# Kernel optimization log

Measured on AMD Instinct MI355X. Metric: run time of the kernel, lower is better.

## Reference

```python
import jax, jax.numpy as jnp
import numpy as np

N, B, F_DIM, K, DEG = 102400, 64, 64, 16, 8
E = N * DEG
PER_G = N // B  # equal-size graphs -> to_dense_batch is a reshape
EPS = 1e-15


def setup_inputs() -> dict:
    key = jax.random.key(0)
    k1, k2, k3, k4 = jax.random.split(key, 4)
    node_attr = jax.random.normal(k1, (N, F_DIM), dtype=jnp.float32)
    W = jax.random.normal(k2, (F_DIM, K), dtype=jnp.float32) * 0.1
    b = jnp.zeros((K,), dtype=jnp.float32)
    row = jax.random.randint(k3, (E,), 0, N)
    # receivers constrained to the sender's graph (block structure)
    col = (row // PER_G) * PER_G + jax.random.randint(k4, (E,), 0, PER_G)
    edge_index = jnp.stack([row, col]).astype(jnp.int32)
    batch = jnp.repeat(jnp.arange(B, dtype=jnp.int32), PER_G)
    return {"node_attr": node_attr, "W": W, "b": b,
            "edge_index": edge_index, "batch": batch, "num_graphs": B}


def reference(node_attr, W, b, edge_index, batch, num_graphs):
    n, f = node_attr.shape
    k = W.shape[1]
    per_g = n // num_graphs
    # selection = softmax(Linear(node_attr))            [N, K]
    sel = jax.nn.softmax(node_attr @ W + b, axis=-1)
    s = sel.reshape(num_graphs, per_g, k)               # to_dense_batch (equal graphs)
    row, col = edge_index[0], edge_index[1]
    # edge_pooling: outer product per edge, scatter-add by graph of sender
    assign_edge = sel[row][:, :, None] * sel[col][:, None, :]       # [E, K, K]
    dense_adj = jax.ops.segment_sum(assign_edge, batch[row], num_segments=num_graphs)  # [B, K, K]
    # normalize_adj (remove_self_loops=False)
    d = jnp.sqrt(dense_adj.sum(-1))[:, None, :] + EPS   # [B, 1, K]
    dense_adj = dense_adj / d / jnp.swapaxes(d, 1, 2)
    # mincut loss
    mincut_num = jnp.trace(dense_adj, axis1=1, axis2=2)             # [B]
    deg = jax.ops.segment_sum(jnp.ones((row.shape[0],), node_attr.dtype), row, num_segments=n)
    d_flat = deg.reshape(num_graphs, per_g)                          # [B, Nmax]
    # trace(S^T diag(d) S) = sum_n d_n * sum_k s_nk^2
    mincut_den = jnp.einsum('bn,bnk,bnk->b', d_flat, s, s)
    mincut_loss = jnp.mean(-(mincut_num / mincut_den))
    # orthogonality loss
    ss = jnp.einsum('bnk,bnl->bkl', s, s)                            # [B, K, K]
    ss_norm = jnp.linalg.norm(ss, axis=(-2, -1), keepdims=True)
    i_s = jnp.eye(k, dtype=ss.dtype)
    ortho = jnp.linalg.norm(ss / ss_norm - i_s / jnp.sqrt(jnp.asarray(k, ss.dtype)), axis=(-2, -1))
    ortho_loss = jnp.mean(ortho)
    # node_pooling: scatter of sel ⊗ node_attr by graph, flattened over (B, K)
    x = node_attr.reshape(num_graphs, per_g, f)
    cluster_node_attr = jnp.einsum('bnk,bnf->bkf', s, x).reshape(num_graphs * k, f)
    return cluster_node_attr, dense_adj, mincut_loss, ortho_loss
```

## Files before the change

kernel.cpp:

```cpp
#include <hip/hip_runtime.h>

#define F_DIMC 64
#define K_DIMC 16
#define NGRAPH 64
#define NXCD 8
#define SX_WAVES 8
#define SX_SPLIT 8
#define NB_SEL 400
#define NB_CHUNK 256
#define NB_ZERO 64
#define CHUNK_I4 800
#define ADJ_BLOCKS 256
#define ADJ_OFF (NGRAPH * K_DIMC * F_DIMC)
#define LOSS_OFF (ADJ_OFF + NGRAPH * K_DIMC * K_DIMC)
#define ZERO_BYTES 394240

typedef __attribute__((ext_vector_type(8))) short s16x8;
typedef __attribute__((ext_vector_type(4))) float f32x4;


__device__ inline unsigned short f2bf(float f) {
    unsigned u = __builtin_bit_cast(unsigned, f);
    u += 0x7fffu + ((u >> 16) & 1u);
    return (unsigned short)(u >> 16);
}

__global__ __launch_bounds__(256) void k_sel_hist(const float* __restrict__ node_attr,
                                                  const float* __restrict__ W,
                                                  const float* __restrict__ bias,
                                                  const int* __restrict__ row,
                                                  float* __restrict__ sel,
                                                  int* __restrict__ blockhist,
                                                  float4* __restrict__ zdst,
                                                  int N, int perG) {
    int t = threadIdx.x;
    if (blockIdx.x < NB_SEL) {
        __shared__ float sW[K_DIMC][F_DIMC];
        __shared__ float sb[K_DIMC];
        for (int idx = t; idx < F_DIMC * K_DIMC; idx += 256) {
            int f = idx / K_DIMC, k = idx % K_DIMC;
            sW[k][f] = W[idx];
        }
        if (t < K_DIMC) sb[t] = bias[t];
        __syncthreads();
        int n = blockIdx.x * 256 + t;
        if (n >= N) return;

        const float4* xr = (const float4*)(node_attr + (size_t)n * F_DIMC);
        float4 x[F_DIMC / 4];
#pragma unroll
        for (int f4 = 0; f4 < F_DIMC / 4; ++f4) x[f4] = xr[f4];

        float logits[K_DIMC];
#pragma unroll
        for (int k = 0; k < K_DIMC; ++k) {
            const float4* wk = (const float4*)&sW[k][0];
            float acc = sb[k];
#pragma unroll
            for (int f4 = 0; f4 < F_DIMC / 4; ++f4) {
                float4 w = wk[f4];
                acc += x[f4].x * w.x + x[f4].y * w.y + x[f4].z * w.z + x[f4].w * w.w;
            }
            logits[k] = acc;
        }
        float m = logits[0];
#pragma unroll
        for (int k = 1; k < K_DIMC; ++k) m = fmaxf(m, logits[k]);
        float sum = 0.f;
#pragma unroll
        for (int k = 0; k < K_DIMC; ++k) {
            float e = __expf(logits[k] - m);
            logits[k] = e;
            sum += e;
        }
        float inv = 1.f / sum;
        float4* sd = (float4*)(sel + (size_t)n * K_DIMC);
#pragma unroll
        for (int k4 = 0; k4 < K_DIMC / 4; ++k4) {
            float4 v;
            v.x = logits[4 * k4 + 0] * inv;
            v.y = logits[4 * k4 + 1] * inv;
            v.z = logits[4 * k4 + 2] * inv;
            v.w = logits[4 * k4 + 3] * inv;
            sd[k4] = v;
        }
    } else if (blockIdx.x < NB_SEL + NB_CHUNK) {
        __shared__ int lh[NGRAPH];
        int h = blockIdx.x - NB_SEL;
        if (t < NGRAPH) lh[t] = 0;
        __syncthreads();
        for (int i = t; i < CHUNK_I4; i += 256) {
            int4 r4 = ((const int4*)row)[h * CHUNK_I4 + i];
            atomicAdd(&lh[r4.x / perG], 1);
            atomicAdd(&lh[r4.y / perG], 1);
            atomicAdd(&lh[r4.z / perG], 1);
            atomicAdd(&lh[r4.w / perG], 1);
        }
        __syncthreads();
        if (t < NGRAPH) blockhist[h * NGRAPH + t] = lh[t];
    } else {
        int z = blockIdx.x - NB_SEL - NB_CHUNK;
        for (int i = z * 256 + t; i < ZERO_BYTES / 16; i += NB_ZERO * 256)
            zdst[i] = make_float4(0.f, 0.f, 0.f, 0.f);
    }
}

__global__ __launch_bounds__(256) void k_chunkscan(const int* __restrict__ blockhist,
                                                   int* __restrict__ chunkbase,
                                                   int* __restrict__ gtot) {
    int g = blockIdx.x;
    int t = threadIdx.x;
    int lane = t & 63;
    int wid = t >> 6;
    int v = blockhist[t * NGRAPH + g];
    int s = v;
#pragma unroll
    for (int d = 1; d < 64; d <<= 1) {
        int o = __shfl_up(s, d);
        if (lane >= d) s += o;
    }
    __shared__ int wsum[4];
    if (lane == 63) wsum[wid] = s;
    __syncthreads();
    int pre = 0;
#pragma unroll
    for (int w = 0; w < 4; ++w) pre += (w < wid) ? wsum[w] : 0;
    int incl = s + pre;
    chunkbase[t * NGRAPH + g] = incl - v;
    if (t == 255) gtot[g] = incl;
}

__global__ __launch_bounds__(256) void k_scatter(const int* __restrict__ row,
                                                 const int* __restrict__ col,
                                                 const int* __restrict__ gtot,
                                                 const int* __restrict__ chunkbase,
                                                 int* __restrict__ offsets,
                                                 uint2* __restrict__ sorted,
                                                 int perG) {
    __shared__ int base_[NGRAPH];
    __shared__ int lcnt[NGRAPH];
    int t = threadIdx.x;
    int h = blockIdx.x;
    if (t < 64) {
        int v = gtot[t];
        int s = v;
#pragma unroll
        for (int d = 1; d < 64; d <<= 1) {
            int o = __shfl_up(s, d);
            if (t >= d) s += o;
        }
        int offs = s - v;
        base_[t] = offs + chunkbase[h * NGRAPH + t];
        lcnt[t] = 0;
        if (h == 0) offsets[t] = offs;
    }
    __syncthreads();
    for (int i = t; i < CHUNK_I4; i += 256) {
        int e4 = h * CHUNK_I4 + i;
        int4 r4 = ((const int4*)row)[e4];
        int4 c4 = ((const int4*)col)[e4];
        int rr[4] = {r4.x, r4.y, r4.z, r4.w};
        int cc[4] = {c4.x, c4.y, c4.z, c4.w};
#pragma unroll
        for (int u = 0; u < 4; ++u) {
            int g = rr[u] / perG;
            int lpos = atomicAdd(&lcnt[g], 1);
            sorted[(size_t)base_[g] + lpos] = make_uint2((unsigned)rr[u], (unsigned)cc[u]);
        }
    }
}

__global__ __launch_bounds__(256) void k_adj(const uint2* __restrict__ sorted,
                                             const int* __restrict__ offsets,
                                             const int* __restrict__ gtot,
                                             const float* __restrict__ sel,
                                             float* __restrict__ dense_raw,
                                             float* __restrict__ den) {
    __shared__ unsigned short At[4][512];
    __shared__ unsigned short Bt[4][512];
    __shared__ float lacc[4][256];
    __shared__ float qred[4];
    int b = blockIdx.x;
    int xcd = b & (NXCD - 1);
    int idx = b >> 3;
    int g = xcd * (NGRAPH / NXCD) + (idx >> 2);
    int split = idx & 3;
    int t = threadIdx.x;
    int wid = t >> 6;
    int lane = t & 63;
    int m = lane & 15;
    int grp = lane >> 4;
    int half8 = (lane & 1) * 8;

    int start = offsets[g];
    int cnt = gtot[g];
    int wslot = split * 4 + wid;
    f32x4 acc = {0.f, 0.f, 0.f, 0.f};
    float qacc = 0.f;
    int nch = (cnt + 31) >> 5;
    for (int ch = wslot; ch < nch; ch += 16) {
        int e0 = ch << 5;
        int eIdx = e0 + (lane >> 1);
        s16x8 av8 = {0, 0, 0, 0, 0, 0, 0, 0};
        s16x8 bv8 = {0, 0, 0, 0, 0, 0, 0, 0};
        if (eIdx < cnt) {
            uint2 pr = sorted[start + eIdx];
            const float4* ra = (const float4*)(sel + (size_t)pr.x * K_DIMC + half8);
            float4 a0 = ra[0], a1 = ra[1];
            qacc += a0.x * a0.x + a0.y * a0.y + a0.z * a0.z + a0.w * a0.w
                  + a1.x * a1.x + a1.y * a1.y + a1.z * a1.z + a1.w * a1.w;
            av8[0] = (short)f2bf(a0.x); av8[1] = (short)f2bf(a0.y);
            av8[2] = (short)f2bf(a0.z); av8[3] = (short)f2bf(a0.w);
            av8[4] = (short)f2bf(a1.x); av8[5] = (short)f2bf(a1.y);
            av8[6] = (short)f2bf(a1.z); av8[7] = (short)f2bf(a1.w);
            const float4* rb = (const float4*)(sel + (size_t)pr.y * K_DIMC + half8);
            float4 b0 = rb[0], b1 = rb[1];
            bv8[0] = (short)f2bf(b0.x); bv8[1] = (short)f2bf(b0.y);
            bv8[2] = (short)f2bf(b0.z); bv8[3] = (short)f2bf(b0.w);
            bv8[4] = (short)f2bf(b1.x); bv8[5] = (short)f2bf(b1.y);
            bv8[6] = (short)f2bf(b1.z); bv8[7] = (short)f2bf(b1.w);
        }
        ((s16x8*)At[wid])[lane] = av8;
        ((s16x8*)Bt[wid])[lane] = bv8;
        s16x8 av, bv;
#pragma unroll
        for (int d = 0; d < 8; ++d) {
            int off = (8 * grp + d) * K_DIMC + m;
            av[d] = (short)At[wid][off];
            bv[d] = (short)Bt[wid][off];
        }
        acc = __builtin_amdgcn_mfma_f32_16x16x32_bf16(av, bv, acc, 0, 0, 0);
    }
#pragma unroll
    for (int d = 0; d < 4; ++d) {
        lacc[wid][(4 * grp + d) * K_DIMC + m] = acc[d];
    }
#pragma unroll
    for (int off = 32; off > 0; off >>= 1) qacc += __shfl_down(qacc, off);
    if (lane == 0) qred[wid] = qacc;
    __syncthreads();
    float s = lacc[0][t] + lacc[1][t] + lacc[2][t] + lacc[3][t];
    atomicAdd(dense_raw + g * 256 + t, s);
    if (t == 0) {
        atomicAdd(den + g, qred[0] + qred[1] + qred[2] + qred[3]);
    }
}

__global__ __launch_bounds__(512) void k_sx(const float* __restrict__ sel,
                                            const float* __restrict__ x,
                                            float* __restrict__ ssbuf,
                                            float* __restrict__ sxbuf, int perG) {
    int g = blockIdx.y;
    int wid = threadIdx.x >> 6;
    int wslot = blockIdx.x * SX_WAVES + wid;
    int lane = threadIdx.x & 63;
    int k = lane >> 2;
    int sub = lane & 3;
    int f0 = sub * 16;
    int j0 = sub * 4;
    float accss[4] = {0.f, 0.f, 0.f, 0.f};
    float accsx[16];
#pragma unroll
    for (int j = 0; j < 16; ++j) accsx[j] = 0.f;
    size_t base = (size_t)g * perG;
    int stride = SX_SPLIT * SX_WAVES;
#pragma unroll 2
    for (int nn = wslot; nn < perG; nn += stride) {
        size_t node = base + nn;
        float a = sel[node * K_DIMC + k];
        float4 s4 = *(const float4*)(sel + node * K_DIMC + j0);
        accss[0] += a * s4.x;
        accss[1] += a * s4.y;
        accss[2] += a * s4.z;
        accss[3] += a * s4.w;
        const float4* xv = (const float4*)(x + node * F_DIMC + f0);
#pragma unroll
        for (int j = 0; j < 4; ++j) {
            float4 v = xv[j];
            accsx[4 * j + 0] += a * v.x;
            accsx[4 * j + 1] += a * v.y;
            accsx[4 * j + 2] += a * v.z;
            accsx[4 * j + 3] += a * v.w;
        }
    }
    __shared__ float lsx[SX_WAVES][K_DIMC * F_DIMC];
    __shared__ float lss[SX_WAVES][256];
#pragma unroll
    for (int j4 = 0; j4 < 4; ++j4) {
        *(float4*)&lsx[wid][k * F_DIMC + f0 + 4 * j4] =
            make_float4(accsx[4 * j4], accsx[4 * j4 + 1], accsx[4 * j4 + 2], accsx[4 * j4 + 3]);
    }
    *(float4*)&lss[wid][k * K_DIMC + j0] = make_float4(accss[0], accss[1], accss[2], accss[3]);
    __syncthreads();
    for (int c = threadIdx.x; c < K_DIMC * F_DIMC; c += 512) {
        float s = 0.f;
#pragma unroll
        for (int w = 0; w < SX_WAVES; ++w) s += lsx[w][c];
        atomicAdd(sxbuf + (size_t)g * (K_DIMC * F_DIMC) + c, s);
    }
    if (threadIdx.x < 256) {
        int c = threadIdx.x;
        float s = 0.f;
#pragma unroll
        for (int w = 0; w < SX_WAVES; ++w) s += lss[w][c];
        atomicAdd(ssbuf + g * 256 + c, s);
    }
}

__global__ __launch_bounds__(256) void k_fin(const float* __restrict__ dense_raw,
                                             const float* __restrict__ ssbuf,
                                             const float* __restrict__ sxbuf,
                                             const float* __restrict__ den,
                                             float* __restrict__ lossws,
                                             int* __restrict__ donecnt,
                                             float* __restrict__ out) {
    int g = blockIdx.x;
    int c = threadIdx.x;
    int k = c >> 4, j = c & 15;
    int lane = threadIdx.x & 63;
    int wid = threadIdx.x >> 6;

    ((float4*)(out + (size_t)g * (K_DIMC * F_DIMC)))[c] =
        ((const float4*)(sxbuf + (size_t)g * (K_DIMC * F_DIMC)))[c];

    float a = dense_raw[g * 256 + c];
    float s = a;
    s += __shfl_xor(s, 1);
    s += __shfl_xor(s, 2);
    s += __shfl_xor(s, 4);
    s += __shfl_xor(s, 8);
    __shared__ float dvrow[K_DIMC];
    if (j == 0) dvrow[k] = sqrtf(s) + 1e-15f;
    __syncthreads();
    float v = a / (dvrow[k] * dvrow[j]);
    out[ADJ_OFF + g * 256 + c] = v;

    float ss = ssbuf[g * 256 + c];
    float tt = (k == j) ? v : 0.f;
    float n2 = ss * ss;
#pragma unroll
    for (int off = 32; off > 0; off >>= 1) {
        tt += __shfl_down(tt, off);
        n2 += __shfl_down(n2, off);
    }
    __shared__ float redt[4], redn[4];
    if (lane == 0) { redt[wid] = tt; redn[wid] = n2; }
    __syncthreads();
    float tr = redt[0] + redt[1] + redt[2] + redt[3];
    float nrm2 = redn[0] + redn[1] + redn[2] + redn[3];
    float invn = 1.f / sqrtf(nrm2);
    float d = ss * invn - ((k == j) ? 0.25f : 0.f);
    float o2 = d * d;
#pragma unroll
    for (int off = 32; off > 0; off >>= 1) o2 += __shfl_down(o2, off);
    __shared__ float redo[4];
    if (lane == 0) redo[wid] = o2;
    __syncthreads();
    if (threadIdx.x == 0) {
        float osum = redo[0] + redo[1] + redo[2] + redo[3];
        float og = sqrtf(osum);
        float mterm = -(tr / den[g]);
        atomicAdd(lossws + 0, mterm * (1.f / NGRAPH));
        atomicAdd(lossws + 1, og * (1.f / NGRAPH));
        __threadfence();
        int old = atomicAdd(donecnt, 1);
        if (old == NGRAPH - 1) {
            float l0 = atomicAdd(lossws + 0, 0.f);
            float l1 = atomicAdd(lossws + 1, 0.f);
            out[LOSS_OFF + 0] = l0;
            out[LOSS_OFF + 1] = l1;
        }
    }
}

extern "C" void kernel_launch(void* const* d_in, const int* in_sizes, int n_in,
                              void* d_out, int out_size, void* d_ws, size_t ws_size,
                              hipStream_t stream) {
    const float* node_attr = (const float*)d_in[0];
    const float* W = (const float*)d_in[1];
    const float* bias = (const float*)d_in[2];
    const int* edge_index = (const int*)d_in[3];
    int N = in_sizes[0] / F_DIMC;
    int E = in_sizes[3] / 2;
    int perG = N / NGRAPH;
    const int* row = edge_index;
    const int* col = edge_index + E;
    float* out = (float*)d_out;
    char* ws = (char*)d_ws;

    float* den = (float*)(ws + 0);
    int* donecnt = (int*)(ws + 256);
    float* lossws = (float*)(ws + 512);
    float* dense_raw = (float*)(ws + 1024);
    float* ssbuf = (float*)(ws + 66560);
    float* sxbuf = (float*)(ws + 132096);
    int* offsets = (int*)(ws + 394240);
    int* gtot = (int*)(ws + 394496);
    int* blockhist = (int*)(ws + 394752);
    int* chunkbase = (int*)(ws + 460288);
    float* sel = (float*)(ws + 525824);
    uint2* sorted = (uint2*)(ws + 7079424);

    k_sel_hist<<<NB_SEL + NB_CHUNK + NB_ZERO, 256, 0, stream>>>(node_attr, W, bias, row, sel,
                                                                blockhist, (float4*)ws, N, perG);
    k_chunkscan<<<NGRAPH, 256, 0, stream>>>(blockhist, chunkbase, gtot);
    k_scatter<<<NB_CHUNK, 256, 0, stream>>>(row, col, gtot, chunkbase, offsets,
                                            sorted, perG);
    k_adj<<<ADJ_BLOCKS, 256, 0, stream>>>(sorted, offsets, gtot, sel, dense_raw, den);
    k_sx<<<dim3(SX_SPLIT, NGRAPH), 512, 0, stream>>>(sel, node_attr, ssbuf, sxbuf, perG);
    k_fin<<<NGRAPH, 256, 0, stream>>>(dense_raw, ssbuf, sxbuf, den, lossws, donecnt, out);
}
```

Baseline: 85.97 us.

## Fuse node-pooling reduction into edge scatter kernel via heterogeneous blocks

Merges the S^T S / S^T X reduction kernel into the edge scatter kernel as additional block roles, interleaving one scatter block with four reduction blocks. This removes a kernel launch and lets the memory-bound reduction overlap with the atomic-heavy scatter. The reduction uses 256-thread blocks with twice as many splits and an XCD-aware graph mapping. Shared memory for both roles is allocated per block, which may reduce occupancy for the scatter blocks.

```diff
diff --git a/kernel.cpp b/kernel.cpp
--- a/kernel.cpp
+++ b/kernel.cpp
@@ -4,8 +4,7 @@
 #define K_DIMC 16
 #define NGRAPH 64
 #define NXCD 8
-#define SX_WAVES 8
-#define SX_SPLIT 8
+#define SX_SPLIT 16
 #define NB_SEL 400
 #define NB_CHUNK 256
 #define NB_ZERO 64
@@ -130,42 +129,104 @@
     if (t == 255) gtot[g] = incl;
 }
 
-__global__ __launch_bounds__(256) void k_scatter(const int* __restrict__ row,
-                                                 const int* __restrict__ col,
-                                                 const int* __restrict__ gtot,
-                                                 const int* __restrict__ chunkbase,
-                                                 int* __restrict__ offsets,
-                                                 uint2* __restrict__ sorted,
-                                                 int perG) {
-    __shared__ int base_[NGRAPH];
-    __shared__ int lcnt[NGRAPH];
+__global__ __launch_bounds__(256) void k_scatter_sx(const int* __restrict__ row,
+                                                    const int* __restrict__ col,
+                                                    const int* __restrict__ gtot,
+                                                    const int* __restrict__ chunkbase,
+                                                    int* __restrict__ offsets,
+                                                    uint2* __restrict__ sorted,
+                                                    const float* __restrict__ sel,
+                                                    const float* __restrict__ x,
+                                                    float* __restrict__ ssbuf,
+                                                    float* __restrict__ sxbuf,
+                                                    int perG) {
+    int b = blockIdx.x;
+    int r5 = b % 5;
     int t = threadIdx.x;
-    int h = blockIdx.x;
-    if (t < 64) {
-        int v = gtot[t];
-        int s = v;
-#pragma unroll
-        for (int d = 1; d < 64; d <<= 1) {
-            int o = __shfl_up(s, d);
-            if (t >= d) s += o;
-        }
-        int offs = s - v;
-        base_[t] = offs + chunkbase[h * NGRAPH + t];
-        lcnt[t] = 0;
-        if (h == 0) offsets[t] = offs;
-    }
-    __syncthreads();
-    for (int i = t; i < CHUNK_I4; i += 256) {
-        int e4 = h * CHUNK_I4 + i;
-        int4 r4 = ((const int4*)row)[e4];
-        int4 c4 = ((const int4*)col)[e4];
-        int rr[4] = {r4.x, r4.y, r4.z, r4.w};
-        int cc[4] = {c4.x, c4.y, c4.z, c4.w};
-#pragma unroll
-        for (int u = 0; u < 4; ++u) {
-            int g = rr[u] / perG;
-            int lpos = atomicAdd(&lcnt[g], 1);
-            sorted[(size_t)base_[g] + lpos] = make_uint2((unsigned)rr[u], (unsigned)cc[u]);
+    if (r5 == 0) {
+        __shared__ int base_[NGRAPH];
+        __shared__ int lcnt[NGRAPH];
+        int h = b / 5;
+        if (t < 64) {
+            int v = gtot[t];
+            int s = v;
+#pragma unroll
+            for (int d = 1; d < 64; d <<= 1) {
+                int o = __shfl_up(s, d);
+                if (t >= d) s += o;
+            }
+            int offs = s - v;
+            base_[t] = offs + chunkbase[h * NGRAPH + t];
+            lcnt[t] = 0;
+            if (h == 0) offsets[t] = offs;
+        }
+        __syncthreads();
+        for (int i = t; i < CHUNK_I4; i += 256) {
+            int e4 = h * CHUNK_I4 + i;
+            int4 r4 = ((const int4*)row)[e4];
+            int4 c4 = ((const int4*)col)[e4];
+            int rr[4] = {r4.x, r4.y, r4.z, r4.w};
+            int cc[4] = {c4.x, c4.y, c4.z, c4.w};
+#pragma unroll
+            for (int u = 0; u < 4; ++u) {
+                int g = rr[u] / perG;
+                int lpos = atomicAdd(&lcnt[g], 1);
+                sorted[(size_t)base_[g] + lpos] = make_uint2((unsigned)rr[u], (unsigned)cc[u]);
+            }
+        }
+    } else {
+        int s = (b / 5) * 4 + (r5 - 1);
+        int xcd = s & (NXCD - 1);
+        int rem = s >> 3;
+        int g = xcd * (NGRAPH / NXCD) + (rem >> 4);
+        int split = rem & (SX_SPLIT - 1);
+        int wid = t >> 6;
+        int wslot = split * 4 + wid;
+        int lane = t & 63;
+        int k = lane >> 2;
+        int sub = lane & 3;
+        int f0 = sub * 16;
+        int j0 = sub * 4;
+        float accss[4] = {0.f, 0.f, 0.f, 0.f};
+        float accsx[16];
+#pragma unroll
+        for (int j = 0; j < 16; ++j) accsx[j] = 0.f;
+        size_t base = (size_t)g * perG;
+#pragma unroll 2
+        for (int nn = wslot; nn < perG; nn += 64) {
+            size_t node = base + nn;
+            float a = sel[node * K_DIMC + k];
+            float4 s4 = *(const float4*)(sel + node * K_DIMC + j0);
+            accss[0] += a * s4.x;
+            accss[1] += a * s4.y;
+            accss[2] += a * s4.z;
+            accss[3] += a * s4.w;
+            const float4* xv = (const float4*)(x + node * F_DIMC + f0);
+#pragma unroll
+            for (int j = 0; j < 4; ++j) {
+                float4 v = xv[j];
+                accsx[4 * j + 0] += a * v.x;
+                accsx[4 * j + 1] += a * v.y;
+                accsx[4 * j + 2] += a * v.z;
+                accsx[4 * j + 3] += a * v.w;
+            }
+        }
+        __shared__ float lsx[4][K_DIMC * F_DIMC];
+        __shared__ float lss[4][256];
+#pragma unroll
+        for (int j4 = 0; j4 < 4; ++j4) {
+            *(float4*)&lsx[wid][k * F_DIMC + f0 + 4 * j4] =
+                make_float4(accsx[4 * j4], accsx[4 * j4 + 1], accsx[4 * j4 + 2], accsx[4 * j4 + 3]);
+        }
+        *(float4*)&lss[wid][k * K_DIMC + j0] = make_float4(accss[0], accss[1], accss[2], accss[3]);
+        __syncthreads();
+        for (int c = t; c < K_DIMC * F_DIMC; c += 256) {
+            float sm = lsx[0][c] + lsx[1][c] + lsx[2][c] + lsx[3][c];
+            atomicAdd(sxbuf + (size_t)g * (K_DIMC * F_DIMC) + c, sm);
+        }
+        {
+            float sm = lss[0][t] + lss[1][t] + lss[2][t] + lss[3][t];
+            atomicAdd(ssbuf + g * 256 + t, sm);
         }
     }
 }
@@ -246,67 +307,6 @@
     }
 }
 
-__global__ __launch_bounds__(512) void k_sx(const float* __restrict__ sel,
-                                            const float* __restrict__ x,
-                                            float* __restrict__ ssbuf,
-                                            float* __restrict__ sxbuf, int perG) {
-    int g = blockIdx.y;
-    int wid = threadIdx.x >> 6;
-    int wslot = blockIdx.x * SX_WAVES + wid;
-    int lane = threadIdx.x & 63;
-    int k = lane >> 2;
-    int sub = lane & 3;
-    int f0 = sub * 16;
-    int j0 = sub * 4;
-    float accss[4] = {0.f, 0.f, 0.f, 0.f};
-    float accsx[16];
-#pragma unroll
-    for (int j = 0; j < 16; ++j) accsx[j] = 0.f;
-    size_t base = (size_t)g * perG;
-    int stride = SX_SPLIT * SX_WAVES;
-#pragma unroll 2
-    for (int nn = wslot; nn < perG; nn += stride) {
-        size_t node = base + nn;
-        float a = sel[node * K_DIMC + k];
-        float4 s4 = *(const float4*)(sel + node * K_DIMC + j0);
-        accss[0] += a * s4.x;
-        accss[1] += a * s4.y;
-        accss[2] += a * s4.z;
-        accss[3] += a * s4.w;
-        const float4* xv = (const float4*)(x + node * F_DIMC + f0);
-#pragma unroll
-        for (int j = 0; j < 4; ++j) {
-            float4 v = xv[j];
-            accsx[4 * j + 0] += a * v.x;
-            accsx[4 * j + 1] += a * v.y;
-            accsx[4 * j + 2] += a * v.z;
-            accsx[4 * j + 3] += a * v.w;
-        }
-    }
-    __shared__ float lsx[SX_WAVES][K_DIMC * F_DIMC];
-    __shared__ float lss[SX_WAVES][256];
-#pragma unroll
-    for (int j4 = 0; j4 < 4; ++j4) {
-        *(float4*)&lsx[wid][k * F_DIMC + f0 + 4 * j4] =
-            make_float4(accsx[4 * j4], accsx[4 * j4 + 1], accsx[4 * j4 + 2], accsx[4 * j4 + 3]);
-    }
-    *(float4*)&lss[wid][k * K_DIMC + j0] = make_float4(accss[0], accss[1], accss[2], accss[3]);
-    __syncthreads();
-    for (int c = threadIdx.x; c < K_DIMC * F_DIMC; c += 512) {
-        float s = 0.f;
-#pragma unroll
-        for (int w = 0; w < SX_WAVES; ++w) s += lsx[w][c];
-        atomicAdd(sxbuf + (size_t)g * (K_DIMC * F_DIMC) + c, s);
-    }
-    if (threadIdx.x < 256) {
-        int c = threadIdx.x;
-        float s = 0.f;
-#pragma unroll
-        for (int w = 0; w < SX_WAVES; ++w) s += lss[w][c];
-        atomicAdd(ssbuf + g * 256 + c, s);
-    }
-}
-
 __global__ __launch_bounds__(256) void k_fin(const float* __restrict__ dense_raw,
                                              const float* __restrict__ ssbuf,
                                              const float* __restrict__ sxbuf,
@@ -404,9 +404,8 @@
     k_sel_hist<<<NB_SEL + NB_CHUNK + NB_ZERO, 256, 0, stream>>>(node_attr, W, bias, row, sel,
                                                                 blockhist, (float4*)ws, N, perG);
     k_chunkscan<<<NGRAPH, 256, 0, stream>>>(blockhist, chunkbase, gtot);
-    k_scatter<<<NB_CHUNK, 256, 0, stream>>>(row, col, gtot, chunkbase, offsets,
-                                            sorted, perG);
+    k_scatter_sx<<<NB_CHUNK * 5, 256, 0, stream>>>(row, col, gtot, chunkbase, offsets,
+                                                   sorted, sel, node_attr, ssbuf, sxbuf, perG);
     k_adj<<<ADJ_BLOCKS, 256, 0, stream>>>(sorted, offsets, gtot, sel, dense_raw, den);
-    k_sx<<<dim3(SX_SPLIT, NGRAPH), 512, 0, stream>>>(sel, node_attr, ssbuf, sxbuf, perG);
     k_fin<<<NGRAPH, 256, 0, stream>>>(dense_raw, ssbuf, sxbuf, den, lossws, donecnt, out);
 }
```

New measurement: 86.33 us. About the same (+0.4%).
